# Optimization experiments

Measured on AMD Instinct MI355X. Metric: run time of the kernel, lower is better.

Reference implementation:

```python
import jax, jax.numpy as jnp
import numpy as np

EPS = 1e-5

def conv1x1(x, w, b):
    # x: [B,C,H,W], w: [O,C], b: [O] -> [B,O,H,W]
    return jnp.einsum('bchw,oc->bohw', x, w) + b[None, :, None, None]

def setup_inputs() -> dict:
    key = jax.random.key(0)
    ks = jax.random.split(key, 12)
    B, C, Ci, H, W = 4, 256, 128, 64, 64
    s = lambda fan_in: 1.0 / np.sqrt(fan_in)
    return {
        'x': jax.random.normal(ks[0], (B, C, H, W), jnp.float32),
        'source': jax.random.normal(ks[1], (B, C, H, W), jnp.float32),
        'g_w': jax.random.normal(ks[2], (Ci, C), jnp.float32) * s(C),
        'g_b': jax.random.normal(ks[3], (Ci,), jnp.float32) * s(C),
        'theta_w': jax.random.normal(ks[4], (Ci, C), jnp.float32) * s(C),
        'theta_b': jax.random.normal(ks[5], (Ci,), jnp.float32) * s(C),
        'phi_w': jax.random.normal(ks[6], (Ci, C), jnp.float32) * s(C),
        'phi_b': jax.random.normal(ks[7], (Ci,), jnp.float32) * s(C),
        'wz_w': jax.random.normal(ks[8], (C, Ci), jnp.float32) * s(Ci),
        'wz_b': jax.random.normal(ks[9], (C,), jnp.float32) * s(Ci),
        'bn_gamma': jax.random.normal(ks[10], (C,), jnp.float32),
        'bn_beta': jax.random.normal(ks[11], (C,), jnp.float32),
    }

def reference(x, source, g_w, g_b, theta_w, theta_b, phi_w, phi_b, wz_w, wz_b, bn_gamma, bn_beta):
    B, C, H, W = source.shape
    Ci = g_w.shape[0]
    N = H * W
    # 1x1 conv embeddings, flattened over spatial dims
    g_x = conv1x1(source, g_w, g_b).reshape(B, Ci, N).transpose(0, 2, 1)      # [B,N,Ci]
    theta_x = conv1x1(x, theta_w, theta_b).reshape(B, Ci, N).transpose(0, 2, 1)  # [B,N,Ci]
    phi_x = conv1x1(source, phi_w, phi_b).reshape(B, Ci, N)                   # [B,Ci,N]
    # embedded-gaussian attention (no scaling, matching original)
    f = jnp.einsum('bnc,bcm->bnm', theta_x, phi_x)          # [B,N,N]
    f_div_C = jax.nn.softmax(f, axis=-1)
    y = jnp.einsum('bnm,bmc->bnc', f_div_C, g_x)            # [B,N,Ci]
    y = y.transpose(0, 2, 1).reshape(B, Ci, H, W)
    # W_z: conv1x1 + BatchNorm2d (training-mode batch statistics)
    w_y = conv1x1(y, wz_w, wz_b)                            # [B,C,H,W]
    mean = jnp.mean(w_y, axis=(0, 2, 3), keepdims=True)
    var = jnp.var(w_y, axis=(0, 2, 3), keepdims=True)
    w_y = (w_y - mean) * jax.lax.rsqrt(var + EPS)
    w_y = w_y * bn_gamma[None, :, None, None] + bn_beta[None, :, None, None]
    return w_y + source
```

## Files before the change

### kernel.cpp

```cpp
#include <hip/hip_runtime.h>
#include <math.h>

#define B_  4
#define C_  256
#define CI_ 128
#define N_  4096
#define D_  128
#define KVSPLIT 4
#define KVQ  (N_ / KVSPLIT)
#define KVT  64
#define NT   (KVQ / KVT)
#define LOG2E 1.4426950408889634f

typedef _Float16 f16;
typedef f16 f16x8 __attribute__((ext_vector_type(8)));
typedef __fp16 fp16x2 __attribute__((ext_vector_type(2)));
typedef float f32x4 __attribute__((ext_vector_type(4)));
typedef unsigned short u16;

__device__ __forceinline__ u16 f2h(float x) {
    union { f16 h; u16 u; } v; v.h = (f16)x; return v.u;
}
__device__ __forceinline__ unsigned pkrtz(float a, float b) {
    union { fp16x2 h; unsigned u; } v;
    v.h = __builtin_amdgcn_cvt_pkrtz(a, b);
    return v.u;
}

__device__ __forceinline__ void gll16(const void* g, void* l) {
    __builtin_amdgcn_global_load_lds(
        (const __attribute__((address_space(1))) void*)g,
        (__attribute__((address_space(3))) void*)l, 16, 0, 0);
}

__global__ __launch_bounds__(256) void embed_kernel(
    const float* __restrict__ x, const float* __restrict__ src,
    const float* __restrict__ g_w, const float* __restrict__ g_b,
    const float* __restrict__ th_w, const float* __restrict__ th_b,
    const float* __restrict__ ph_w, const float* __restrict__ ph_b,
    u16* __restrict__ th, u16* __restrict__ ph, u16* __restrict__ gt)
{
    __shared__ u16 xh[2][64 * 40];

    const int n0 = blockIdx.x * 64, b = blockIdx.y, which = blockIdx.z;
    const float* in   = which ? src  : x;
    const float* wm   = which ? ph_w : th_w;
    const float* bias = which ? ph_b : th_b;
    const float wscale = which ? 1.0f : LOG2E;

    const int t = threadIdx.x, lane = t & 63, wv = t >> 6;
    const int lq = lane & 15, lh = lane >> 4;
    const int mf0 = wv * 2, cq = t >> 6;

    f32x4 accp[2][4], accg[2][4];
#pragma unroll
    for (int m = 0; m < 2; ++m) {
        float b0 = bias[16 * (mf0 + m) + 4 * lh + 0] * wscale;
        float b1 = bias[16 * (mf0 + m) + 4 * lh + 1] * wscale;
        float b2 = bias[16 * (mf0 + m) + 4 * lh + 2] * wscale;
        float b3 = bias[16 * (mf0 + m) + 4 * lh + 3] * wscale;
#pragma unroll
        for (int s = 0; s < 4; ++s) accp[m][s] = (f32x4){b0, b1, b2, b3};
        if (which) {
            float g0 = g_b[16 * (mf0 + m) + 4 * lh + 0];
            float g1 = g_b[16 * (mf0 + m) + 4 * lh + 1];
            float g2 = g_b[16 * (mf0 + m) + 4 * lh + 2];
            float g3 = g_b[16 * (mf0 + m) + 4 * lh + 3];
#pragma unroll
            for (int s = 0; s < 4; ++s) accg[m][s] = (f32x4){g0, g1, g2, g3};
        }
    }

    const float* colbase = in + (size_t)b * C_ * N_ + n0;

    float iv[2][8];
    f16x8 wp_[2][2], wg_[2][2];

    auto load_inputs = [&](int slot, int k) {
        const int c0 = k * 32;
#pragma unroll
        for (int p = 0; p < 2; ++p) {
            int cl = 16 * p + 4 * cq;
#pragma unroll
            for (int e = 0; e < 4; ++e)
                iv[slot][4 * p + e] = colbase[(size_t)(c0 + cl + e) * N_ + lane];
        }
    };
    auto load_weights = [&](int slot, int k) {
        const int c0 = k * 32;
#pragma unroll
        for (int m = 0; m < 2; ++m) {
            const float* wp = wm + (size_t)(16 * (mf0 + m) + lq) * C_ + c0 + 8 * lh;
            float4 a = *(const float4*)wp;
            float4 bq = *(const float4*)(wp + 4);
            wp_[slot][m][0] = (f16)(a.x * wscale);  wp_[slot][m][1] = (f16)(a.y * wscale);
            wp_[slot][m][2] = (f16)(a.z * wscale);  wp_[slot][m][3] = (f16)(a.w * wscale);
            wp_[slot][m][4] = (f16)(bq.x * wscale); wp_[slot][m][5] = (f16)(bq.y * wscale);
            wp_[slot][m][6] = (f16)(bq.z * wscale); wp_[slot][m][7] = (f16)(bq.w * wscale);
            if (which) {
                const float* wg = g_w + (size_t)(16 * (mf0 + m) + lq) * C_ + c0 + 8 * lh;
                float4 ga = *(const float4*)wg;
                float4 gq = *(const float4*)(wg + 4);
                wg_[slot][m][0] = (f16)ga.x;  wg_[slot][m][1] = (f16)ga.y;
                wg_[slot][m][2] = (f16)ga.z;  wg_[slot][m][3] = (f16)ga.w;
                wg_[slot][m][4] = (f16)gq.x;  wg_[slot][m][5] = (f16)gq.y;
                wg_[slot][m][6] = (f16)gq.z;  wg_[slot][m][7] = (f16)gq.w;
            }
        }
    };
    auto write_lds = [&](int slot) {
#pragma unroll
        for (int p = 0; p < 2; ++p) {
            int cl = 16 * p + 4 * cq;
            union { f16 h[4]; ushort4 u; } cv;
            cv.h[0] = (f16)iv[slot][4 * p + 0];
            cv.h[1] = (f16)iv[slot][4 * p + 1];
            cv.h[2] = (f16)iv[slot][4 * p + 2];
            cv.h[3] = (f16)iv[slot][4 * p + 3];
            *(ushort4*)&xh[slot][lane * 40 + cl] = cv.u;
        }
    };

    load_inputs(0, 0);
    load_weights(0, 0);
    write_lds(0);
    load_inputs(1, 1);
    load_weights(1, 1);

#pragma unroll
    for (int k = 0; k < 8; ++k) {
        const int cur = k & 1, nxt = cur ^ 1;
        __syncthreads();
        if (k < 7) write_lds(nxt);
        if (k < 6) load_inputs(cur, k + 2);

#pragma unroll
        for (int s = 0; s < 4; ++s) {
            f16x8 xf = *(const f16x8*)&xh[cur][(16 * s + lq) * 40 + 8 * lh];
#pragma unroll
            for (int m = 0; m < 2; ++m) {
                accp[m][s] = __builtin_amdgcn_mfma_f32_16x16x32_f16(wp_[cur][m], xf, accp[m][s], 0, 0, 0);
                if (which)
                    accg[m][s] = __builtin_amdgcn_mfma_f32_16x16x32_f16(wg_[cur][m], xf, accg[m][s], 0, 0, 0);
            }
        }
        if (k < 6) load_weights(cur, k + 2);
    }

    u16* op = (which ? ph : th) + (size_t)b * N_ * CI_;
#pragma unroll
    for (int m = 0; m < 2; ++m)
#pragma unroll
        for (int s = 0; s < 4; ++s) {
            ushort4 pk = {f2h(accp[m][s][0]), f2h(accp[m][s][1]),
                          f2h(accp[m][s][2]), f2h(accp[m][s][3])};
            *(ushort4*)(op + (size_t)(n0 + 16 * s + lq) * CI_ + 16 * (mf0 + m) + 4 * lh) = pk;
        }
    if (which) {
        u16* gb2 = gt + (size_t)b * CI_ * N_;
#pragma unroll
        for (int m = 0; m < 2; ++m)
#pragma unroll
            for (int s = 0; s < 4; ++s)
#pragma unroll
                for (int r = 0; r < 4; ++r)
                    gb2[(size_t)(16 * (mf0 + m) + 4 * lh + r) * N_ + n0 + 16 * s + lq] =
                        f2h(accg[m][s][r]);
    }
}

__global__ __launch_bounds__(256, 2) void attn_kernel(
    const u16* __restrict__ th, const u16* __restrict__ ph,
    const u16* __restrict__ gt, u16* __restrict__ part, float* __restrict__ ml)
{
    __shared__ u16 Ks[2][KVT * 128];
    __shared__ u16 Vt[2][64 * 128];
    __shared__ unsigned Pl[4][16 * 36];

    const int n0 = blockIdx.x * 128, b = blockIdx.y, sp = blockIdx.z;
    const int t = threadIdx.x, wv = t >> 6, lane = t & 63;
    const int lq = lane & 15, lh = lane >> 4;
    const int q0w = n0 + wv * 32;

    const u16* kb = ph + ((size_t)b * N_ + (size_t)sp * KVQ) * D_;
    const u16* vb = gt + (size_t)b * D_ * N_ + sp * KVQ;

    f16x8 qf[2][4];
#pragma unroll
    for (int qs = 0; qs < 2; ++qs) {
        const u16* qp = th + ((size_t)b * N_ + q0w + 16 * qs + lq) * D_ + 8 * lh;
#pragma unroll
        for (int c = 0; c < 4; ++c) qf[qs][c] = *(const f16x8*)(qp + 32 * c);
    }

    f32x4 Ot[2][8];
#pragma unroll
    for (int qs = 0; qs < 2; ++qs)
#pragma unroll
        for (int j = 0; j < 8; ++j) Ot[qs][j] = (f32x4){0.f, 0.f, 0.f, 0.f};
    float m_run[2] = {-INFINITY, -INFINITY};
    float l_run[2] = {0.f, 0.f};

    auto stage = [&](int buf, int it) {
        const int kv0 = it * KVT;
#pragma unroll
        for (int ii = 0; ii < 4; ++ii) {
            int i = 4 * wv + ii;
            int rr = 4 * i + (lane >> 4);
            const u16* g = kb + (size_t)(kv0 + rr) * D_ + (((lane & 15) ^ (rr & 7)) * 8);
            gll16(g, &Ks[buf][i * 512]);
        }
#pragma unroll
        for (int jj = 0; jj < 4; ++jj) {
            int j = 4 * wv + jj;
            int r = 4 * j + (lane >> 4);
            int s = lane & 15;
            int c6 = s ^ (r & 7);
            int dd = 2 * r + (c6 >> 3);
            const u16* g = vb + (size_t)dd * N_ + kv0 + (c6 & 7) * 8;
            gll16(g, &Vt[buf][j * 512]);
        }
    };

    stage(0, 0);
    for (int it = 0; it < NT; ++it) {
        __syncthreads();
        if (it + 1 < NT) stage((it + 1) & 1, it + 1);
        const u16* K = Ks[it & 1];
        const u16* V = Vt[it & 1];

        f32x4 S[2][4];
#pragma unroll
        for (int qs = 0; qs < 2; ++qs)
#pragma unroll
            for (int tt = 0; tt < 4; ++tt) S[qs][tt] = (f32x4){0.f, 0.f, 0.f, 0.f};
#pragma unroll
        for (int c = 0; c < 4; ++c)
#pragma unroll
            for (int tt = 0; tt < 4; ++tt) {
                int row = 16 * tt + lq;
                f16x8 kf = *(const f16x8*)&K[row * 128 + ((32 * c + 8 * lh) ^ ((row & 7) << 3))];
                S[0][tt] = __builtin_amdgcn_mfma_f32_16x16x32_f16(kf, qf[0][c], S[0][tt], 0, 0, 0);
                S[1][tt] = __builtin_amdgcn_mfma_f32_16x16x32_f16(kf, qf[1][c], S[1][tt], 0, 0, 0);
            }

        f16x8 pf[2][2];
#pragma unroll
        for (int qs = 0; qs < 2; ++qs) {
            float mx = -INFINITY;
#pragma unroll
            for (int tt = 0; tt < 4; ++tt)
#pragma unroll
                for (int r = 0; r < 4; ++r) mx = fmaxf(mx, S[qs][tt][r]);
            mx = fmaxf(mx, __shfl_xor(mx, 16));
            mx = fmaxf(mx, __shfl_xor(mx, 32));
            if (!__all(mx <= m_run[qs])) {
                float mn = fmaxf(m_run[qs], mx);
                float al = exp2f(m_run[qs] - mn);
                m_run[qs] = mn;
                l_run[qs] *= al;
#pragma unroll
                for (int j = 0; j < 8; ++j) Ot[qs][j] *= al;
            }
            float p[4][4];
            float ls = 0.f;
#pragma unroll
            for (int tt = 0; tt < 4; ++tt)
#pragma unroll
                for (int r = 0; r < 4; ++r) {
                    p[tt][r] = exp2f(S[qs][tt][r] - m_run[qs]);
                    ls += p[tt][r];
                }
            ls += __shfl_xor(ls, 16);
            ls += __shfl_xor(ls, 32);
            l_run[qs] += ls;

            unsigned* pw = &Pl[wv][lq * 36];
#pragma unroll
            for (int tt = 0; tt < 4; ++tt) {
                uint2 wpair;
                wpair.x = pkrtz(p[tt][0], p[tt][1]);
                wpair.y = pkrtz(p[tt][2], p[tt][3]);
                *(uint2*)(pw + 8 * tt + 2 * lh) = wpair;
            }
            union { uint4 u; f16x8 v; } pu0, pu1;
            pu0.u = *(const uint4*)(pw + 4 * lh);
            pu1.u = *(const uint4*)(pw + 16 + 4 * lh);
            pf[qs][0] = pu0.v;
            pf[qs][1] = pu1.v;
        }

#pragma unroll
        for (int cc = 0; cc < 2; ++cc)
#pragma unroll
            for (int j = 0; j < 8; ++j) {
                int r = 8 * j + (lq >> 1);
                int slot = (((lq & 1) << 3) | (4 * cc + lh)) ^ (r & 7);
                f16x8 vf = *(const f16x8*)&V[r * 128 + slot * 8];
                Ot[0][j] = __builtin_amdgcn_mfma_f32_16x16x32_f16(vf, pf[0][cc], Ot[0][j], 0, 0, 0);
                Ot[1][j] = __builtin_amdgcn_mfma_f32_16x16x32_f16(vf, pf[1][cc], Ot[1][j], 0, 0, 0);
            }
    }

#pragma unroll
    for (int qs = 0; qs < 2; ++qs) {
        u16* pb = part + (((size_t)sp * B_ + b) * N_ + q0w + 16 * qs + lq) * D_;
#pragma unroll
        for (int j = 0; j < 8; ++j) {
            uint2 pk2;
            pk2.x = pkrtz(Ot[qs][j][0], Ot[qs][j][1]);
            pk2.y = pkrtz(Ot[qs][j][2], Ot[qs][j][3]);
            *(uint2*)(pb + 16 * j + 4 * lh) = pk2;
        }
        if (lh == 0) {
            float* mp = ml + (((size_t)sp * B_ + b) * N_ + q0w + 16 * qs + lq) * 2;
            mp[0] = m_run[qs];
            mp[1] = l_run[qs];
        }
    }
}

__global__ __launch_bounds__(512) void wz_kernel(
    const u16* __restrict__ part, const float* __restrict__ ml,
    const float* __restrict__ wz_w, const float* __restrict__ wz_b,
    u16* __restrict__ w_y, float* __restrict__ sums8)
{
    __shared__ u16 ylds[64 * 128];
    const int n0 = blockIdx.x * 64, b = blockIdx.y;
    const int t = threadIdx.x, lane = t & 63, wv = t >> 6;
    const int lq = lane & 15, lh = lane >> 4;
    const int rep = blockIdx.x & 7;

    f16x8 wf[4][2];
#pragma unroll
    for (int k = 0; k < 4; ++k)
#pragma unroll
        for (int mm = 0; mm < 2; ++mm) {
            const float* wp = wz_w + (size_t)(16 * (2 * wv + mm) + lq) * CI_ + 32 * k + 8 * lh;
            float4 a = *(const float4*)wp;
            float4 bq = *(const float4*)(wp + 4);
            wf[k][mm][0] = (f16)a.x;  wf[k][mm][1] = (f16)a.y;
            wf[k][mm][2] = (f16)a.z;  wf[k][mm][3] = (f16)a.w;
            wf[k][mm][4] = (f16)bq.x; wf[k][mm][5] = (f16)bq.y;
            wf[k][mm][6] = (f16)bq.z; wf[k][mm][7] = (f16)bq.w;
        }

#pragma unroll
    for (int i = 0; i < 2; ++i) {
        int flat = i * 512 + t;
        int row = flat >> 4, s = flat & 15;
        int q = n0 + row;
        float2 mls[KVSPLIT];
        float m = -INFINITY;
#pragma unroll
        for (int sp = 0; sp < KVSPLIT; ++sp) {
            mls[sp] = *(const float2*)(ml + (((size_t)sp * B_ + b) * N_ + q) * 2);
            m = fmaxf(m, mls[sp].x);
        }
        float wts[KVSPLIT], denom = 0.f;
#pragma unroll
        for (int sp = 0; sp < KVSPLIT; ++sp) {
            wts[sp] = exp2f(mls[sp].x - m);
            denom += wts[sp] * mls[sp].y;
        }
        float inv = 1.f / denom;
        float acc8[8];
#pragma unroll
        for (int e = 0; e < 8; ++e) acc8[e] = 0.f;
#pragma unroll
        for (int sp = 0; sp < KVSPLIT; ++sp) {
            f16x8 o = *(const f16x8*)(part + (((size_t)sp * B_ + b) * N_ + q) * D_ + 8 * s);
#pragma unroll
            for (int e = 0; e < 8; ++e) acc8[e] += wts[sp] * (float)o[e];
        }
        union { f16 h[8]; f16x8 v; } mv;
#pragma unroll
        for (int e = 0; e < 8; ++e) mv.h[e] = (f16)(acc8[e] * inv);
        *(f16x8*)&ylds[row * 128 + 8 * (s ^ (row & 7))] = mv.v;
    }
    __syncthreads();

    f32x4 acc[2][4];
#pragma unroll
    for (int mm = 0; mm < 2; ++mm) {
        float b0 = wz_b[16 * (2 * wv + mm) + 4 * lh + 0];
        float b1 = wz_b[16 * (2 * wv + mm) + 4 * lh + 1];
        float b2 = wz_b[16 * (2 * wv + mm) + 4 * lh + 2];
        float b3 = wz_b[16 * (2 * wv + mm) + 4 * lh + 3];
#pragma unroll
        for (int s = 0; s < 4; ++s) acc[mm][s] = (f32x4){b0, b1, b2, b3};
    }

#pragma unroll
    for (int k = 0; k < 4; ++k)
#pragma unroll
        for (int s = 0; s < 4; ++s) {
            int row = 16 * s + lq;
            f16x8 yf = *(const f16x8*)&ylds[row * 128 + 8 * ((4 * k + lh) ^ (row & 7))];
#pragma unroll
            for (int mm = 0; mm < 2; ++mm)
                acc[mm][s] = __builtin_amdgcn_mfma_f32_16x16x32_f16(wf[k][mm], yf, acc[mm][s], 0, 0, 0);
        }

#pragma unroll
    for (int mm = 0; mm < 2; ++mm) {
        int cb = 16 * (2 * wv + mm) + 4 * lh;
#pragma unroll
        for (int s = 0; s < 4; ++s) {
            int n = n0 + 16 * s + lq;
#pragma unroll
            for (int r = 0; r < 4; ++r)
                w_y[((size_t)b * C_ + cb + r) * N_ + n] = f2h(acc[mm][s][r]);
        }
#pragma unroll
        for (int r = 0; r < 4; ++r) {
            float sv = acc[mm][0][r] + acc[mm][1][r] + acc[mm][2][r] + acc[mm][3][r];
            float qv = acc[mm][0][r] * acc[mm][0][r] + acc[mm][1][r] * acc[mm][1][r]
                     + acc[mm][2][r] * acc[mm][2][r] + acc[mm][3][r] * acc[mm][3][r];
#pragma unroll
            for (int d = 1; d < 16; d <<= 1) {
                sv += __shfl_xor(sv, d);
                qv += __shfl_xor(qv, d);
            }
            if (lq == 0) {
                atomicAdd(&sums8[rep * 512 + cb + r], sv);
                atomicAdd(&sums8[rep * 512 + C_ + cb + r], qv);
            }
        }
    }
}

__global__ __launch_bounds__(256) void final_kernel(
    const u16* __restrict__ w_y, const float* __restrict__ src,
    const float* __restrict__ gamma, const float* __restrict__ beta,
    const float* __restrict__ sums8, float* __restrict__ out)
{
    const float invN = 1.0f / (float)(B_ * N_);
    size_t i8 = ((size_t)blockIdx.x * blockDim.x + threadIdx.x) * 8;
    if (i8 >= (size_t)B_ * C_ * N_) return;
    int c = (int)((i8 / N_) % C_);
    float ssum = 0.f, ssq = 0.f;
#pragma unroll
    for (int rp = 0; rp < 8; ++rp) {
        ssum += sums8[rp * 512 + c];
        ssq  += sums8[rp * 512 + C_ + c];
    }
    float mean  = ssum * invN;
    float var   = ssq * invN - mean * mean;
    float scale = rsqrtf(var + 1e-5f) * gamma[c];
    float bb    = beta[c];
    f16x8 w = *(const f16x8*)(w_y + i8);
    float4 s0 = *(const float4*)(src + i8);
    float4 s1 = *(const float4*)(src + i8 + 4);
    float4 o0, o1;
    o0.x = ((float)w[0] - mean) * scale + bb + s0.x;
    o0.y = ((float)w[1] - mean) * scale + bb + s0.y;
    o0.z = ((float)w[2] - mean) * scale + bb + s0.z;
    o0.w = ((float)w[3] - mean) * scale + bb + s0.w;
    o1.x = ((float)w[4] - mean) * scale + bb + s1.x;
    o1.y = ((float)w[5] - mean) * scale + bb + s1.y;
    o1.z = ((float)w[6] - mean) * scale + bb + s1.z;
    o1.w = ((float)w[7] - mean) * scale + bb + s1.w;
    *(float4*)(out + i8)     = o0;
    *(float4*)(out + i8 + 4) = o1;
}

extern "C" void kernel_launch(void* const* d_in, const int* in_sizes, int n_in,
                              void* d_out, int out_size, void* d_ws, size_t ws_size,
                              hipStream_t stream)
{
    const float* x     = (const float*)d_in[0];
    const float* src   = (const float*)d_in[1];
    const float* g_w   = (const float*)d_in[2];
    const float* g_b   = (const float*)d_in[3];
    const float* th_w  = (const float*)d_in[4];
    const float* th_b  = (const float*)d_in[5];
    const float* ph_w  = (const float*)d_in[6];
    const float* ph_b  = (const float*)d_in[7];
    const float* wz_w  = (const float*)d_in[8];
    const float* wz_b  = (const float*)d_in[9];
    const float* gamma = (const float*)d_in[10];
    const float* beta  = (const float*)d_in[11];

    char* ws = (char*)d_ws;
    u16*   th    = (u16*)(ws + (0u  << 20));
    u16*   ph    = (u16*)(ws + (4u  << 20));
    u16*   gt    = (u16*)(ws + (8u  << 20));
    u16*   part  = (u16*)(ws + (12u << 20));
    float* mlbuf = (float*)(ws + (28u << 20));
    u16*   w_y   = (u16*)(ws + (0u  << 20));
    float* sums8 = (float*)(ws + (28u << 20) + (1u << 19));

    hipMemsetAsync(sums8, 0, 8 * 2 * C_ * sizeof(float), stream);

    embed_kernel<<<dim3(64, 4, 2), 256, 0, stream>>>(
        x, src, g_w, g_b, th_w, th_b, ph_w, ph_b, th, ph, gt);
    attn_kernel<<<dim3(N_ / 128, B_, KVSPLIT), 256, 0, stream>>>(
        th, ph, gt, part, mlbuf);
    wz_kernel<<<dim3(N_ / 64, B_), 512, 0, stream>>>(part, mlbuf, wz_w, wz_b, w_y, sums8);
    final_kernel<<<2048, 256, 0, stream>>>(w_y, src, gamma, beta, sums8, (float*)d_out);
}
```

Measured before the change: 105.0 us.

## Split g embedding into its own grid slice and raise MFMA wave priority in attention

The embed kernel's z grid dimension grows from 2 to 3, so the g projection runs in separate blocks instead of sharing the phi blocks. This removes the imbalance where phi blocks did twice the MFMA work and held twice the accumulator registers, at the cost of reading source a second time. The attention kernel also wraps its two MFMA phases in s_setprio(1)/s_setprio(0), so waves issuing matrix ops get scheduling priority over waves doing softmax work.

```diff
diff --git a/kernel.cpp b/kernel.cpp
--- a/kernel.cpp
+++ b/kernel.cpp
@@ -43,16 +43,16 @@
     __shared__ u16 xh[2][64 * 40];
 
     const int n0 = blockIdx.x * 64, b = blockIdx.y, which = blockIdx.z;
-    const float* in   = which ? src  : x;
-    const float* wm   = which ? ph_w : th_w;
-    const float* bias = which ? ph_b : th_b;
-    const float wscale = which ? 1.0f : LOG2E;
+    const float* in   = which ? src : x;
+    const float* wm   = (which == 0) ? th_w : (which == 1 ? ph_w : g_w);
+    const float* bias = (which == 0) ? th_b : (which == 1 ? ph_b : g_b);
+    const float wscale = (which == 0) ? LOG2E : 1.0f;
 
     const int t = threadIdx.x, lane = t & 63, wv = t >> 6;
     const int lq = lane & 15, lh = lane >> 4;
     const int mf0 = wv * 2, cq = t >> 6;
 
-    f32x4 accp[2][4], accg[2][4];
+    f32x4 acc[2][4];
 #pragma unroll
     for (int m = 0; m < 2; ++m) {
         float b0 = bias[16 * (mf0 + m) + 4 * lh + 0] * wscale;
@@ -60,21 +60,13 @@
         float b2 = bias[16 * (mf0 + m) + 4 * lh + 2] * wscale;
         float b3 = bias[16 * (mf0 + m) + 4 * lh + 3] * wscale;
 #pragma unroll
-        for (int s = 0; s < 4; ++s) accp[m][s] = (f32x4){b0, b1, b2, b3};
-        if (which) {
-            float g0 = g_b[16 * (mf0 + m) + 4 * lh + 0];
-            float g1 = g_b[16 * (mf0 + m) + 4 * lh + 1];
-            float g2 = g_b[16 * (mf0 + m) + 4 * lh + 2];
-            float g3 = g_b[16 * (mf0 + m) + 4 * lh + 3];
-#pragma unroll
-            for (int s = 0; s < 4; ++s) accg[m][s] = (f32x4){g0, g1, g2, g3};
-        }
+        for (int s = 0; s < 4; ++s) acc[m][s] = (f32x4){b0, b1, b2, b3};
     }
 
     const float* colbase = in + (size_t)b * C_ * N_ + n0;
 
     float iv[2][8];
-    f16x8 wp_[2][2], wg_[2][2];
+    f16x8 wf_[2][2];
 
     auto load_inputs = [&](int slot, int k) {
         const int c0 = k * 32;
@@ -93,19 +85,10 @@
             const float* wp = wm + (size_t)(16 * (mf0 + m) + lq) * C_ + c0 + 8 * lh;
             float4 a = *(const float4*)wp;
             float4 bq = *(const float4*)(wp + 4);
-            wp_[slot][m][0] = (f16)(a.x * wscale);  wp_[slot][m][1] = (f16)(a.y * wscale);
-            wp_[slot][m][2] = (f16)(a.z * wscale);  wp_[slot][m][3] = (f16)(a.w * wscale);
-            wp_[slot][m][4] = (f16)(bq.x * wscale); wp_[slot][m][5] = (f16)(bq.y * wscale);
-            wp_[slot][m][6] = (f16)(bq.z * wscale); wp_[slot][m][7] = (f16)(bq.w * wscale);
-            if (which) {
-                const float* wg = g_w + (size_t)(16 * (mf0 + m) + lq) * C_ + c0 + 8 * lh;
-                float4 ga = *(const float4*)wg;
-                float4 gq = *(const float4*)(wg + 4);
-                wg_[slot][m][0] = (f16)ga.x;  wg_[slot][m][1] = (f16)ga.y;
-                wg_[slot][m][2] = (f16)ga.z;  wg_[slot][m][3] = (f16)ga.w;
-                wg_[slot][m][4] = (f16)gq.x;  wg_[slot][m][5] = (f16)gq.y;
-                wg_[slot][m][6] = (f16)gq.z;  wg_[slot][m][7] = (f16)gq.w;
-            }
+            wf_[slot][m][0] = (f16)(a.x * wscale);  wf_[slot][m][1] = (f16)(a.y * wscale);
+            wf_[slot][m][2] = (f16)(a.z * wscale);  wf_[slot][m][3] = (f16)(a.w * wscale);
+            wf_[slot][m][4] = (f16)(bq.x * wscale); wf_[slot][m][5] = (f16)(bq.y * wscale);
+            wf_[slot][m][6] = (f16)(bq.z * wscale); wf_[slot][m][7] = (f16)(bq.w * wscale);
         }
     };
     auto write_lds = [&](int slot) {
@@ -138,25 +121,23 @@
         for (int s = 0; s < 4; ++s) {
             f16x8 xf = *(const f16x8*)&xh[cur][(16 * s + lq) * 40 + 8 * lh];
 #pragma unroll
-            for (int m = 0; m < 2; ++m) {
-                accp[m][s] = __builtin_amdgcn_mfma_f32_16x16x32_f16(wp_[cur][m], xf, accp[m][s], 0, 0, 0);
-                if (which)
-                    accg[m][s] = __builtin_amdgcn_mfma_f32_16x16x32_f16(wg_[cur][m], xf, accg[m][s], 0, 0, 0);
-            }
+            for (int m = 0; m < 2; ++m)
+                acc[m][s] = __builtin_amdgcn_mfma_f32_16x16x32_f16(wf_[cur][m], xf, acc[m][s], 0, 0, 0);
         }
         if (k < 6) load_weights(cur, k + 2);
     }
 
-    u16* op = (which ? ph : th) + (size_t)b * N_ * CI_;
-#pragma unroll
-    for (int m = 0; m < 2; ++m)
-#pragma unroll
-        for (int s = 0; s < 4; ++s) {
-            ushort4 pk = {f2h(accp[m][s][0]), f2h(accp[m][s][1]),
-                          f2h(accp[m][s][2]), f2h(accp[m][s][3])};
-            *(ushort4*)(op + (size_t)(n0 + 16 * s + lq) * CI_ + 16 * (mf0 + m) + 4 * lh) = pk;
-        }
-    if (which) {
+    if (which < 2) {
+        u16* op = (which == 0 ? th : ph) + (size_t)b * N_ * CI_;
+#pragma unroll
+        for (int m = 0; m < 2; ++m)
+#pragma unroll
+            for (int s = 0; s < 4; ++s) {
+                ushort4 pk = {f2h(acc[m][s][0]), f2h(acc[m][s][1]),
+                              f2h(acc[m][s][2]), f2h(acc[m][s][3])};
+                *(ushort4*)(op + (size_t)(n0 + 16 * s + lq) * CI_ + 16 * (mf0 + m) + 4 * lh) = pk;
+            }
+    } else {
         u16* gb2 = gt + (size_t)b * CI_ * N_;
 #pragma unroll
         for (int m = 0; m < 2; ++m)
@@ -165,7 +146,7 @@
 #pragma unroll
                 for (int r = 0; r < 4; ++r)
                     gb2[(size_t)(16 * (mf0 + m) + 4 * lh + r) * N_ + n0 + 16 * s + lq] =
-                        f2h(accg[m][s][r]);
+                        f2h(acc[m][s][r]);
     }
 }
 
@@ -234,6 +215,7 @@
         for (int qs = 0; qs < 2; ++qs)
 #pragma unroll
             for (int tt = 0; tt < 4; ++tt) S[qs][tt] = (f32x4){0.f, 0.f, 0.f, 0.f};
+        __builtin_amdgcn_s_setprio(1);
 #pragma unroll
         for (int c = 0; c < 4; ++c)
 #pragma unroll
@@ -243,6 +225,7 @@
                 S[0][tt] = __builtin_amdgcn_mfma_f32_16x16x32_f16(kf, qf[0][c], S[0][tt], 0, 0, 0);
                 S[1][tt] = __builtin_amdgcn_mfma_f32_16x16x32_f16(kf, qf[1][c], S[1][tt], 0, 0, 0);
             }
+        __builtin_amdgcn_s_setprio(0);
 
         f16x8 pf[2][2];
 #pragma unroll
@@ -290,6 +273,7 @@
             pf[qs][1] = pu1.v;
         }
 
+        __builtin_amdgcn_s_setprio(1);
 #pragma unroll
         for (int cc = 0; cc < 2; ++cc)
 #pragma unroll
@@ -300,6 +284,7 @@
                 Ot[0][j] = __builtin_amdgcn_mfma_f32_16x16x32_f16(vf, pf[0][cc], Ot[0][j], 0, 0, 0);
                 Ot[1][j] = __builtin_amdgcn_mfma_f32_16x16x32_f16(vf, pf[1][cc], Ot[1][j], 0, 0, 0);
             }
+        __builtin_amdgcn_s_setprio(0);
     }
 
 #pragma unroll
@@ -493,7 +478,7 @@
 
     hipMemsetAsync(sums8, 0, 8 * 2 * C_ * sizeof(float), stream);
 
-    embed_kernel<<<dim3(64, 4, 2), 256, 0, stream>>>(
+    embed_kernel<<<dim3(64, 4, 3), 256, 0, stream>>>(
         x, src, g_w, g_b, th_w, th_b, ph_w, ph_b, th, ph, gt);
     attn_kernel<<<dim3(N_ / 128, B_, KVSPLIT), 256, 0, stream>>>(
         th, ph, gt, part, mlbuf);
```

After: 105.1 us. Within noise of the previous version (+0.1%).
